# Kernel tuning notes

Hardware: AMD Instinct MI355X
Metric: run time of the kernel (lower is better)

The kernel has to match this reference:

```python
import jax, jax.numpy as jnp
import numpy as np

N = 50000      # nodes
E = 800000     # edges
C = 128        # dim_feat / channels
D = 256        # dim_dense
OUT = 2        # dim_out
L = 5          # num_layers - 1 GCN2Conv layers
ALPHA = 0.1    # main_param -> GCN2Conv alpha; theta=None -> beta=1.0
SLOPE = 0.01   # LeakyReLU default negative slope


def setup_inputs() -> dict:
    key = jax.random.key(0)
    ks = jax.random.split(key, 6)
    x = jax.random.normal(ks[0], (N, C), jnp.float32)
    edge_index = jax.random.randint(ks[1], (2, E), 0, N, jnp.int32)
    conv_weights = jax.random.normal(ks[2], (L, C, C), jnp.float32) * (1.0 / np.sqrt(C))
    w_dense = jax.random.normal(ks[3], (C, D), jnp.float32) * (1.0 / np.sqrt(C))
    b_dense = jnp.zeros((D,), jnp.float32)
    w_out = jax.random.normal(ks[4], (D, OUT), jnp.float32) * (1.0 / np.sqrt(D))
    b_out = jnp.zeros((OUT,), jnp.float32)
    return dict(x=x, edge_index=edge_index, conv_weights=conv_weights,
                w_dense=w_dense, b_dense=b_dense, w_out=w_out, b_out=b_out)


def _gcn_norm(edge_index, num_nodes):
    """Symmetric gcn_norm with self-loops: returns row, col, D^-1/2 * D^-1/2 edge weights."""
    loop = jnp.arange(num_nodes, dtype=edge_index.dtype)
    row = jnp.concatenate([edge_index[0], loop])  # sources
    col = jnp.concatenate([edge_index[1], loop])  # targets (aggregation index)
    ones = jnp.ones(row.shape[0], jnp.float32)
    deg = jax.ops.segment_sum(ones, col, num_segments=num_nodes)
    dinv = jnp.where(deg > 0, jax.lax.rsqrt(jnp.maximum(deg, 1e-12)), 0.0)
    return row, col, dinv[row] * dinv[col]


def reference(x, edge_index, conv_weights, w_dense, b_dense, w_out, b_out):
    num_nodes = x.shape[0]
    row, col, norm = _gcn_norm(edge_index, num_nodes)
    x0 = x
    for l in range(conv_weights.shape[0]):
        # propagate: h[i] = sum_{j->i} norm * x[j]   (gather -> scatter-add)
        h = jax.ops.segment_sum(norm[:, None] * x[row], col, num_segments=num_nodes)
        # GCN2Conv with shared_weights=True, beta=1 (theta=None): out = ((1-a)h + a*x0) @ W
        out = (1.0 - ALPHA) * h + ALPHA * x0
        x = jax.nn.leaky_relu(out @ conv_weights[l], negative_slope=SLOPE)
    x = x @ w_dense + b_dense
    return x @ w_out + b_out
```

## Files before the change

### kernel.cpp

```cpp
#include <hip/hip_runtime.h>
#include <hip/hip_fp16.h>

#define C 128
#define NOUT 2
#define ALPHA 0.1f
#define SLOPE 0.01f
#define ZP 136

typedef _Float16 half4v __attribute__((ext_vector_type(4)));
typedef float float4v __attribute__((ext_vector_type(4)));


__global__ void count_kernel(const int* __restrict__ col, int* __restrict__ cnt, int E) {
    int e = blockIdx.x * 256 + threadIdx.x;
    if (e < E) atomicAdd(&cnt[col[e]], 1);
}

__global__ __launch_bounds__(1024) void scanA_kernel(const int* __restrict__ cnt,
                                                     int* __restrict__ offs,
                                                     int* __restrict__ bsum,
                                                     float* __restrict__ dinv, int n) {
    __shared__ int wsum[16];
    int t = threadIdx.x, lane = t & 63, wv = t >> 6;
    int i = blockIdx.x * 1024 + t;
    int v = (i < n) ? cnt[i] : 0;
    if (i < n) dinv[i] = rsqrtf((float)(v + 1));
    int sc = v;
    #pragma unroll
    for (int d = 1; d < 64; d <<= 1) {
        int u = __shfl_up(sc, d);
        if (lane >= d) sc += u;
    }
    if (lane == 63) wsum[wv] = sc;
    __syncthreads();
    int woff = 0;
    #pragma unroll
    for (int j = 0; j < 16; ++j) woff += (j < wv) ? wsum[j] : 0;
    if (i < n) offs[i] = woff + sc - v;
    if (t == 0) {
        int tot = 0;
        #pragma unroll
        for (int j = 0; j < 16; ++j) tot += wsum[j];
        bsum[blockIdx.x] = tot;
    }
}

__global__ __launch_bounds__(1024) void scanB_kernel(const int* __restrict__ bsum,
                                                     int* __restrict__ bbase, int nb) {
    __shared__ int wsum[16];
    int t = threadIdx.x, lane = t & 63, wv = t >> 6;
    int v = (t < nb) ? bsum[t] : 0;
    int sc = v;
    #pragma unroll
    for (int d = 1; d < 64; d <<= 1) {
        int u = __shfl_up(sc, d);
        if (lane >= d) sc += u;
    }
    if (lane == 63) wsum[wv] = sc;
    __syncthreads();
    int woff = 0;
    #pragma unroll
    for (int j = 0; j < 16; ++j) woff += (j < wv) ? wsum[j] : 0;
    if (t < nb) bbase[t] = woff + sc - v;
}

__global__ void scanC_kernel(int* __restrict__ offs, int* __restrict__ cursor,
                             const int* __restrict__ bbase, int n, int E) {
    int i = blockIdx.x * 256 + threadIdx.x;
    if (i < n) {
        int o = offs[i] + bbase[i >> 10];
        offs[i] = o;
        cursor[i] = o;
    }
    if (i == n) offs[n] = E;
}

__global__ void fill_kernel(const int* __restrict__ row, const int* __restrict__ col,
                            const float* __restrict__ dinv, int* __restrict__ cursor,
                            int2* __restrict__ csr, int E) {
    int e = blockIdx.x * 256 + threadIdx.x;
    if (e >= E) return;
    int r = row[e], c = col[e];
    int pos = atomicAdd(&cursor[c], 1);
    int2 m;
    m.x = r;
    m.y = __float_as_int(dinv[r] * dinv[c]);
    csr[pos] = m;
}

__global__ __launch_bounds__(256) void convert_kernel(const float* __restrict__ x,
                                                      __half* __restrict__ xh, int n) {
    int g = blockIdx.x * 256 + threadIdx.x;
    if (g >= n * 32) return;
    float4 v = ((const float4*)x)[g];
    union { __half2 h; unsigned u; } a, b;
    a.h = __float22half2_rn(make_float2(v.x, v.y));
    b.h = __float22half2_rn(make_float2(v.z, v.w));
    ((uint2*)xh)[g] = make_uint2(a.u, b.u);
}

__global__ void wtc_kernel(const float* __restrict__ W, _Float16* __restrict__ WT, int total) {
    int idx = blockIdx.x * 256 + threadIdx.x;
    if (idx >= total) return;
    int l = idx >> 14, rem = idx & 16383;
    int nrow = rem >> 7, kk = rem & 127;
    WT[idx] = (_Float16)W[(l << 14) + kk * C + nrow];
}

__global__ void wdc_kernel(const float* __restrict__ wd, _Float16* __restrict__ WDT) {
    int idx = blockIdx.x * 256 + threadIdx.x;
    if (idx >= 256 * C) return;
    int nrow = idx >> 7, kk = idx & 127;
    WDT[idx] = (_Float16)wd[kk * 256 + nrow];
}

__device__ __forceinline__ void accum8(float* a, uint4 q, float w) {
    union { unsigned u; __half2 h; } c;
    float2 f;
    c.u = q.x; f = __half22float2(c.h); a[0] += w * f.x; a[1] += w * f.y;
    c.u = q.y; f = __half22float2(c.h); a[2] += w * f.x; a[3] += w * f.y;
    c.u = q.z; f = __half22float2(c.h); a[4] += w * f.x; a[5] += w * f.y;
    c.u = q.w; f = __half22float2(c.h); a[6] += w * f.x; a[7] += w * f.y;
}

__device__ __forceinline__ uint4 pack8(const float* a) {
    union { __half2 h; unsigned u; } c0, c1, c2, c3;
    c0.h = __float22half2_rn(make_float2(a[0], a[1]));
    c1.h = __float22half2_rn(make_float2(a[2], a[3]));
    c2.h = __float22half2_rn(make_float2(a[4], a[5]));
    c3.h = __float22half2_rn(make_float2(a[6], a[7]));
    return make_uint4(c0.u, c1.u, c2.u, c3.u);
}

__global__ __launch_bounds__(256) void agg_kernel(
    const __half* __restrict__ xc, const int* __restrict__ offs,
    const int2* __restrict__ csr, const float* __restrict__ dinv,
    __half* __restrict__ h, int n)
{
    int node = blockIdx.x * 4 + (threadIdx.x >> 6);
    if (node >= n) return;
    int lane = threadIdx.x & 63;
    int eslot = lane >> 4, cg = lane & 15;
    const uint4* x4 = (const uint4*)xc;
    float a0[8] = {}, a1[8] = {}, a2[8] = {}, a3[8] = {};
    int beg = offs[node], end = offs[node + 1];
    int k = beg + eslot;
    for (; k + 12 < end; k += 16) {
        int2 m0 = csr[k], m1 = csr[k + 4], m2 = csr[k + 8], m3 = csr[k + 12];
        uint4 q0 = x4[(size_t)m0.x * 16 + cg];
        uint4 q1 = x4[(size_t)m1.x * 16 + cg];
        uint4 q2 = x4[(size_t)m2.x * 16 + cg];
        uint4 q3 = x4[(size_t)m3.x * 16 + cg];
        accum8(a0, q0, __int_as_float(m0.y));
        accum8(a1, q1, __int_as_float(m1.y));
        accum8(a2, q2, __int_as_float(m2.y));
        accum8(a3, q3, __int_as_float(m3.y));
    }
    for (; k < end; k += 4) {
        int2 m = csr[k];
        uint4 q = x4[(size_t)m.x * 16 + cg];
        accum8(a0, q, __int_as_float(m.y));
    }
    #pragma unroll
    for (int j = 0; j < 8; ++j) a0[j] += a1[j] + a2[j] + a3[j];
    #pragma unroll
    for (int j = 0; j < 8; ++j) {
        a0[j] += __shfl_xor(a0[j], 16);
        a0[j] += __shfl_xor(a0[j], 32);
    }
    if (eslot == 0) {
        float di = dinv[node], sw = di * di;
        uint4 qs = x4[(size_t)node * 16 + cg];
        accum8(a0, qs, sw);
        ((uint4*)h)[(size_t)node * 16 + cg] = pack8(a0);
    }
}

__global__ __launch_bounds__(256) void layer_mfma(
    const __half* __restrict__ hbuf, const __half* __restrict__ x0h,
    const _Float16* __restrict__ WT, __half* __restrict__ xn, int n)
{
    __shared__ _Float16 zl[64 * ZP];
    __shared__ _Float16 ol[64 * ZP];
    int i0 = blockIdx.x * 64;
    int t = threadIdx.x;
    int w = t >> 6, lane = t & 63;
    int c = lane & 15, g = lane >> 4;

    const uint4* h4 = (const uint4*)hbuf;
    const uint4* x4 = (const uint4*)x0h;
    for (int p = t; p < 64 * 16; p += 256) {
        int r = p >> 4, c8 = p & 15;
        uint4 zv = make_uint4(0, 0, 0, 0);
        if (i0 + r < n) {
            uint4 hv = h4[(size_t)(i0 + r) * 16 + c8];
            uint4 xv = x4[(size_t)(i0 + r) * 16 + c8];
            const __half2* hp = (const __half2*)&hv;
            const __half2* xp = (const __half2*)&xv;
            __half2* zp = (__half2*)&zv;
            #pragma unroll
            for (int j = 0; j < 4; ++j) {
                float2 hf = __half22float2(hp[j]);
                float2 xf = __half22float2(xp[j]);
                zp[j] = __float22half2_rn(make_float2(
                    (1.f - ALPHA) * hf.x + ALPHA * xf.x,
                    (1.f - ALPHA) * hf.y + ALPHA * xf.y));
            }
        }
        *(uint4*)&zl[r * ZP + c8 * 8] = zv;
    }

    half4v bf[8][2];
    #pragma unroll
    for (int kb = 0; kb < 8; ++kb)
        #pragma unroll
        for (int nt = 0; nt < 2; ++nt)
            bf[kb][nt] = *(const half4v*)&WT[((w * 2 + nt) * 16 + c) * C + kb * 16 + 4 * g];

    __syncthreads();

    #pragma unroll
    for (int m = 0; m < 4; ++m) {
        const _Float16* arow = &zl[(m * 16 + c) * ZP];
        half4v af[8];
        #pragma unroll
        for (int kb = 0; kb < 8; ++kb) af[kb] = *(const half4v*)&arow[kb * 16 + 4 * g];
        float4v acc0 = (float4v)0.f, acc1 = (float4v)0.f;
        #pragma unroll
        for (int kb = 0; kb < 8; ++kb) {
            acc0 = __builtin_amdgcn_mfma_f32_16x16x16f16(af[kb], bf[kb][0], acc0, 0, 0, 0);
            acc1 = __builtin_amdgcn_mfma_f32_16x16x16f16(af[kb], bf[kb][1], acc1, 0, 0, 0);
        }
        #pragma unroll
        for (int r = 0; r < 4; ++r) {
            float v0 = acc0[r]; v0 = v0 > 0.f ? v0 : SLOPE * v0;
            float v1 = acc1[r]; v1 = v1 > 0.f ? v1 : SLOPE * v1;
            ol[(m * 16 + 4 * g + r) * ZP + (w * 2 + 0) * 16 + c] = (_Float16)v0;
            ol[(m * 16 + 4 * g + r) * ZP + (w * 2 + 1) * 16 + c] = (_Float16)v1;
        }
    }
    __syncthreads();
    for (int p = t; p < 64 * 16; p += 256) {
        int r = p >> 4, c8 = p & 15;
        int node = i0 + r;
        if (node < n)
            ((uint4*)xn)[(size_t)node * 16 + c8] = *(uint4*)&ol[r * ZP + c8 * 8];
    }
}

__global__ __launch_bounds__(256) void dense_mfma(
    const __half* __restrict__ xin, const _Float16* __restrict__ WDT,
    const float* __restrict__ bd, const float* __restrict__ wo,
    const float* __restrict__ bo, float* __restrict__ out, int n)
{
    __shared__ _Float16 xl[64 * ZP];
    __shared__ float pp[64][4][2];
    int i0 = blockIdx.x * 64;
    int t = threadIdx.x;
    int w = t >> 6, lane = t & 63;
    int c = lane & 15, g = lane >> 4;

    const uint4* g4 = (const uint4*)xin;
    for (int p = t; p < 64 * 16; p += 256) {
        int r = p >> 4, c8 = p & 15;
        uint4 v = make_uint4(0, 0, 0, 0);
        if (i0 + r < n) v = g4[(size_t)(i0 + r) * 16 + c8];
        *(uint4*)&xl[r * ZP + c8 * 8] = v;
    }

    half4v bf[8][4];
    #pragma unroll
    for (int kb = 0; kb < 8; ++kb)
        #pragma unroll
        for (int nt = 0; nt < 4; ++nt)
            bf[kb][nt] = *(const half4v*)&WDT[((w * 4 + nt) * 16 + c) * C + kb * 16 + 4 * g];
    float bdv[4], wo0[4], wo1[4];
    #pragma unroll
    for (int nt = 0; nt < 4; ++nt) {
        int coln = (w * 4 + nt) * 16 + c;
        bdv[nt] = bd[coln];
        wo0[nt] = wo[coln * 2 + 0];
        wo1[nt] = wo[coln * 2 + 1];
    }

    __syncthreads();

    #pragma unroll
    for (int m = 0; m < 4; ++m) {
        const _Float16* arow = &xl[(m * 16 + c) * ZP];
        half4v af[8];
        #pragma unroll
        for (int kb = 0; kb < 8; ++kb) af[kb] = *(const half4v*)&arow[kb * 16 + 4 * g];
        float4v acc[4];
        #pragma unroll
        for (int nt = 0; nt < 4; ++nt) acc[nt] = (float4v)0.f;
        #pragma unroll
        for (int kb = 0; kb < 8; ++kb) {
            #pragma unroll
            for (int nt = 0; nt < 4; ++nt)
                acc[nt] = __builtin_amdgcn_mfma_f32_16x16x16f16(af[kb], bf[kb][nt], acc[nt], 0, 0, 0);
        }
        float p0[4] = {0.f, 0.f, 0.f, 0.f}, p1[4] = {0.f, 0.f, 0.f, 0.f};
        #pragma unroll
        for (int nt = 0; nt < 4; ++nt) {
            #pragma unroll
            for (int r = 0; r < 4; ++r) {
                float hv = acc[nt][r] + bdv[nt];
                p0[r] += hv * wo0[nt];
                p1[r] += hv * wo1[nt];
            }
        }
        #pragma unroll
        for (int ms = 1; ms <= 8; ms <<= 1) {
            #pragma unroll
            for (int r = 0; r < 4; ++r) {
                p0[r] += __shfl_xor(p0[r], ms);
                p1[r] += __shfl_xor(p1[r], ms);
            }
        }
        if (c == 0) {
            #pragma unroll
            for (int r = 0; r < 4; ++r) {
                pp[m * 16 + 4 * g + r][w][0] = p0[r];
                pp[m * 16 + 4 * g + r][w][1] = p1[r];
            }
        }
    }
    __syncthreads();
    if (t < 128) {
        int r = t >> 1, o = t & 1;
        int node = i0 + r;
        if (node < n) {
            float s = pp[r][0][o] + pp[r][1][o] + pp[r][2][o] + pp[r][3][o];
            out[(size_t)node * NOUT + o] = s + bo[o];
        }
    }
}

extern "C" void kernel_launch(void* const* d_in, const int* in_sizes, int n_in,
                              void* d_out, int out_size, void* d_ws, size_t ws_size,
                              hipStream_t stream) {
    const float* x0    = (const float*)d_in[0];
    const int*   ei    = (const int*)d_in[1];
    const float* convW = (const float*)d_in[2];
    const float* wd    = (const float*)d_in[3];
    const float* bd    = (const float*)d_in[4];
    const float* wo    = (const float*)d_in[5];
    const float* bo    = (const float*)d_in[6];
    float* out = (float*)d_out;

    int N = in_sizes[0] / C;
    int E = in_sizes[1] / 2;
    int L = in_sizes[2] / (C * C);
    const int* row = ei;
    const int* col = ei + E;
    int NB = (N + 1023) / 1024;

    char* p = (char*)d_ws;
    auto alloc = [&](size_t bytes) {
        char* r = p;
        p += (bytes + 255) & ~(size_t)255;
        return r;
    };
    int*      cnt    = (int*)alloc((size_t)N * 4);
    int*      offs   = (int*)alloc((size_t)(N + 1) * 4);
    int*      cursor = (int*)alloc((size_t)N * 4);
    int*      bsum   = (int*)alloc((size_t)NB * 4);
    int*      bbase  = (int*)alloc((size_t)NB * 4);
    int2*     csr    = (int2*)alloc((size_t)E * 8);
    float*    dinv   = (float*)alloc((size_t)N * 4);
    __half*   x0h    = (__half*)alloc((size_t)N * C * 2);
    __half*   bufA   = (__half*)alloc((size_t)N * C * 2);
    __half*   bufB   = (__half*)alloc((size_t)N * C * 2);
    _Float16* WT     = (_Float16*)alloc((size_t)L * C * C * 2);
    _Float16* WDT    = (_Float16*)alloc((size_t)256 * C * 2);

    hipMemsetAsync(cnt, 0, (size_t)N * 4, stream);
    count_kernel<<<(E + 255) / 256, 256, 0, stream>>>(col, cnt, E);
    scanA_kernel<<<NB, 1024, 0, stream>>>(cnt, offs, bsum, dinv, N);
    scanB_kernel<<<1, 1024, 0, stream>>>(bsum, bbase, NB);
    scanC_kernel<<<(N + 256) / 256, 256, 0, stream>>>(offs, cursor, bbase, N, E);
    fill_kernel<<<(E + 255) / 256, 256, 0, stream>>>(row, col, dinv, cursor, csr, E);
    convert_kernel<<<(N * 32 + 255) / 256, 256, 0, stream>>>(x0, x0h, N);
    int wtot = L * C * C;
    wtc_kernel<<<(wtot + 255) / 256, 256, 0, stream>>>(convW, WT, wtot);
    wdc_kernel<<<(256 * C + 255) / 256, 256, 0, stream>>>(wd, WDT);

    const __half* xc = x0h;
    for (int l = 0; l < L; ++l) {
        __half* hbuf = (l & 1) ? bufB : bufA;
        agg_kernel<<<(N + 3) / 4, 256, 0, stream>>>(xc, offs, csr, dinv, hbuf, N);
        layer_mfma<<<(N + 63) / 64, 256, 0, stream>>>(hbuf, x0h,
                                                      WT + (size_t)l * C * C, hbuf, N);
        xc = hbuf;
    }
    dense_mfma<<<(N + 63) / 64, 256, 0, stream>>>(xc, WDT, bd, wo, bo, out, N);
}
```

Before: 411.9 us.

## Pack CSR entries into 32-bit words and fuse x0 residual into aggregation

Each CSR entry shrinks from an int2 (index plus fp32 norm) to one 32-bit word holding a 16-bit source index and an fp16 norm, halving edge-metadata traffic in every aggregation pass. The alpha-weighted mix with x0 moves from the layer GEMM kernel into the aggregation epilogue, so the GEMM loads one input instead of two. The fill kernel now handles four edges per thread. Packing the index into 16 bits assumes fewer than 65536 nodes, and the fp16 norm loses precision.

```diff
diff --git a/kernel.cpp b/kernel.cpp
--- a/kernel.cpp
+++ b/kernel.cpp
@@ -77,15 +77,32 @@
 
 __global__ void fill_kernel(const int* __restrict__ row, const int* __restrict__ col,
                             const float* __restrict__ dinv, int* __restrict__ cursor,
-                            int2* __restrict__ csr, int E) {
-    int e = blockIdx.x * 256 + threadIdx.x;
-    if (e >= E) return;
-    int r = row[e], c = col[e];
-    int pos = atomicAdd(&cursor[c], 1);
-    int2 m;
-    m.x = r;
-    m.y = __float_as_int(dinv[r] * dinv[c]);
-    csr[pos] = m;
+                            unsigned* __restrict__ csr, int E) {
+    int base = blockIdx.x * 1024 + threadIdx.x;
+    int r[4], c[4];
+    bool v[4];
+    #pragma unroll
+    for (int j = 0; j < 4; ++j) {
+        int e = base + j * 256;
+        v[j] = e < E;
+        r[j] = v[j] ? row[e] : 0;
+        c[j] = v[j] ? col[e] : 0;
+    }
+    float nr[4];
+    #pragma unroll
+    for (int j = 0; j < 4; ++j) nr[j] = dinv[r[j]] * dinv[c[j]];
+    int pos[4];
+    #pragma unroll
+    for (int j = 0; j < 4; ++j)
+        pos[j] = v[j] ? atomicAdd(&cursor[c[j]], 1) : 0;
+    #pragma unroll
+    for (int j = 0; j < 4; ++j) {
+        if (v[j]) {
+            union { __half h; unsigned short u; } nh;
+            nh.h = __float2half_rn(nr[j]);
+            csr[pos[j]] = ((unsigned)r[j] << 16) | (unsigned)nh.u;
+        }
+    }
 }
 
 __global__ __launch_bounds__(256) void convert_kernel(const float* __restrict__ x,
@@ -132,10 +149,16 @@
     return make_uint4(c0.u, c1.u, c2.u, c3.u);
 }
 
+__device__ __forceinline__ float norm_of(unsigned m) {
+    union { unsigned short u; __half h; } nh;
+    nh.u = (unsigned short)(m & 0xffffu);
+    return __half2float(nh.h);
+}
+
 __global__ __launch_bounds__(256) void agg_kernel(
-    const __half* __restrict__ xc, const int* __restrict__ offs,
-    const int2* __restrict__ csr, const float* __restrict__ dinv,
-    __half* __restrict__ h, int n)
+    const __half* __restrict__ xc, const __half* __restrict__ x0h,
+    const int* __restrict__ offs, const unsigned* __restrict__ csr,
+    const float* __restrict__ dinv, __half* __restrict__ z, int n)
 {
     int node = blockIdx.x * 4 + (threadIdx.x >> 6);
     if (node >= n) return;
@@ -146,20 +169,20 @@
     int beg = offs[node], end = offs[node + 1];
     int k = beg + eslot;
     for (; k + 12 < end; k += 16) {
-        int2 m0 = csr[k], m1 = csr[k + 4], m2 = csr[k + 8], m3 = csr[k + 12];
-        uint4 q0 = x4[(size_t)m0.x * 16 + cg];
-        uint4 q1 = x4[(size_t)m1.x * 16 + cg];
-        uint4 q2 = x4[(size_t)m2.x * 16 + cg];
-        uint4 q3 = x4[(size_t)m3.x * 16 + cg];
-        accum8(a0, q0, __int_as_float(m0.y));
-        accum8(a1, q1, __int_as_float(m1.y));
-        accum8(a2, q2, __int_as_float(m2.y));
-        accum8(a3, q3, __int_as_float(m3.y));
+        unsigned m0 = csr[k], m1 = csr[k + 4], m2 = csr[k + 8], m3 = csr[k + 12];
+        uint4 q0 = x4[(size_t)(m0 >> 16) * 16 + cg];
+        uint4 q1 = x4[(size_t)(m1 >> 16) * 16 + cg];
+        uint4 q2 = x4[(size_t)(m2 >> 16) * 16 + cg];
+        uint4 q3 = x4[(size_t)(m3 >> 16) * 16 + cg];
+        accum8(a0, q0, norm_of(m0));
+        accum8(a1, q1, norm_of(m1));
+        accum8(a2, q2, norm_of(m2));
+        accum8(a3, q3, norm_of(m3));
     }
     for (; k < end; k += 4) {
-        int2 m = csr[k];
-        uint4 q = x4[(size_t)m.x * 16 + cg];
-        accum8(a0, q, __int_as_float(m.y));
+        unsigned m = csr[k];
+        uint4 q = x4[(size_t)(m >> 16) * 16 + cg];
+        accum8(a0, q, norm_of(m));
     }
     #pragma unroll
     for (int j = 0; j < 8; ++j) a0[j] += a1[j] + a2[j] + a3[j];
@@ -172,13 +195,19 @@
         float di = dinv[node], sw = di * di;
         uint4 qs = x4[(size_t)node * 16 + cg];
         accum8(a0, qs, sw);
-        ((uint4*)h)[(size_t)node * 16 + cg] = pack8(a0);
+        uint4 q0x = ((const uint4*)x0h)[(size_t)node * 16 + cg];
+        float xr[8] = {};
+        accum8(xr, q0x, 1.f);
+        float zz[8];
+        #pragma unroll
+        for (int j = 0; j < 8; ++j) zz[j] = (1.f - ALPHA) * a0[j] + ALPHA * xr[j];
+        ((uint4*)z)[(size_t)node * 16 + cg] = pack8(zz);
     }
 }
 
 __global__ __launch_bounds__(256) void layer_mfma(
-    const __half* __restrict__ hbuf, const __half* __restrict__ x0h,
-    const _Float16* __restrict__ WT, __half* __restrict__ xn, int n)
+    const __half* __restrict__ zin, const _Float16* __restrict__ WT,
+    __half* __restrict__ xn, int n)
 {
     __shared__ _Float16 zl[64 * ZP];
     __shared__ _Float16 ol[64 * ZP];
@@ -187,26 +216,11 @@
     int w = t >> 6, lane = t & 63;
     int c = lane & 15, g = lane >> 4;
 
-    const uint4* h4 = (const uint4*)hbuf;
-    const uint4* x4 = (const uint4*)x0h;
+    const uint4* z4 = (const uint4*)zin;
     for (int p = t; p < 64 * 16; p += 256) {
         int r = p >> 4, c8 = p & 15;
         uint4 zv = make_uint4(0, 0, 0, 0);
-        if (i0 + r < n) {
-            uint4 hv = h4[(size_t)(i0 + r) * 16 + c8];
-            uint4 xv = x4[(size_t)(i0 + r) * 16 + c8];
-            const __half2* hp = (const __half2*)&hv;
-            const __half2* xp = (const __half2*)&xv;
-            __half2* zp = (__half2*)&zv;
-            #pragma unroll
-            for (int j = 0; j < 4; ++j) {
-                float2 hf = __half22float2(hp[j]);
-                float2 xf = __half22float2(xp[j]);
-                zp[j] = __float22half2_rn(make_float2(
-                    (1.f - ALPHA) * hf.x + ALPHA * xf.x,
-                    (1.f - ALPHA) * hf.y + ALPHA * xf.y));
-            }
-        }
+        if (i0 + r < n) zv = z4[(size_t)(i0 + r) * 16 + c8];
         *(uint4*)&zl[r * ZP + c8 * 8] = zv;
     }
 
@@ -367,11 +381,11 @@
     int*      cursor = (int*)alloc((size_t)N * 4);
     int*      bsum   = (int*)alloc((size_t)NB * 4);
     int*      bbase  = (int*)alloc((size_t)NB * 4);
-    int2*     csr    = (int2*)alloc((size_t)E * 8);
+    unsigned* csr    = (unsigned*)alloc((size_t)E * 4);
     float*    dinv   = (float*)alloc((size_t)N * 4);
     __half*   x0h    = (__half*)alloc((size_t)N * C * 2);
     __half*   bufA   = (__half*)alloc((size_t)N * C * 2);
-    __half*   bufB   = (__half*)alloc((size_t)N * C * 2);
+    __half*   zbuf   = (__half*)alloc((size_t)N * C * 2);
     _Float16* WT     = (_Float16*)alloc((size_t)L * C * C * 2);
     _Float16* WDT    = (_Float16*)alloc((size_t)256 * C * 2);
 
@@ -380,7 +394,7 @@
     scanA_kernel<<<NB, 1024, 0, stream>>>(cnt, offs, bsum, dinv, N);
     scanB_kernel<<<1, 1024, 0, stream>>>(bsum, bbase, NB);
     scanC_kernel<<<(N + 256) / 256, 256, 0, stream>>>(offs, cursor, bbase, N, E);
-    fill_kernel<<<(E + 255) / 256, 256, 0, stream>>>(row, col, dinv, cursor, csr, E);
+    fill_kernel<<<(E + 1023) / 1024, 256, 0, stream>>>(row, col, dinv, cursor, csr, E);
     convert_kernel<<<(N * 32 + 255) / 256, 256, 0, stream>>>(x0, x0h, N);
     int wtot = L * C * C;
     wtc_kernel<<<(wtot + 255) / 256, 256, 0, stream>>>(convW, WT, wtot);
@@ -388,11 +402,10 @@
 
     const __half* xc = x0h;
     for (int l = 0; l < L; ++l) {
-        __half* hbuf = (l & 1) ? bufB : bufA;
-        agg_kernel<<<(N + 3) / 4, 256, 0, stream>>>(xc, offs, csr, dinv, hbuf, N);
-        layer_mfma<<<(N + 63) / 64, 256, 0, stream>>>(hbuf, x0h,
-                                                      WT + (size_t)l * C * C, hbuf, N);
-        xc = hbuf;
+        agg_kernel<<<(N + 3) / 4, 256, 0, stream>>>(xc, x0h, offs, csr, dinv, zbuf, N);
+        layer_mfma<<<(N + 63) / 64, 256, 0, stream>>>(zbuf, WT + (size_t)l * C * C,
+                                                      bufA, N);
+        xc = bufA;
     }
     dense_mfma<<<(N + 63) / 64, 256, 0, stream>>>(xc, WDT, bd, wo, bo, out, N);
 }
```

Measured after the change: 411.6 us. Within noise of the previous version (-0.1%).
